# Performance work log

Measured on AMD Instinct MI355X. Metric: run time of the kernel, lower is better.

The kernel has to match this reference:

```python
import jax, jax.numpy as jnp
import numpy as np

H = 16  # n_heads
D = 1024  # embed_dim == input_dim
FF = 4 * D
EPS = 1e-5  # torch LayerNorm default


def layer_norm(x, g, b):
    m = x.mean(-1, keepdims=True)
    v = x.var(-1, keepdims=True)
    return (x - m) / jnp.sqrt(v + EPS) * g + b


def setup_inputs() -> dict:
    key = jax.random.key(0)
    ks = jax.random.split(key, 8)
    s = lambda k, sh: (jax.random.normal(k, sh, jnp.float32) * 0.02)
    return {
        "kq": jax.random.normal(ks[0], (4, 2048, 512), jnp.float32),
        "v": jax.random.normal(ks[1], (4, 2048, 512), jnp.float32),
        "Wk": s(ks[2], (D, D)), "bk": jnp.zeros((D,), jnp.float32),
        "Wq": s(ks[3], (D, D)), "bq": jnp.zeros((D,), jnp.float32),
        "Wv": s(ks[4], (D, D)), "bv": jnp.zeros((D,), jnp.float32),
        "W1": s(ks[5], (FF, D)), "b1": jnp.zeros((FF,), jnp.float32),
        "W2": s(ks[6], (D, FF)), "b2": jnp.zeros((D,), jnp.float32),
        "g1": jnp.ones((D,), jnp.float32), "be1": jnp.zeros((D,), jnp.float32),
        "g2": jnp.ones((D,), jnp.float32), "be2": jnp.zeros((D,), jnp.float32),
    }


def reference(kq, v, Wk, bk, Wq, bq, Wv, bv, W1, b1, W2, b2, g1, be1, g2, be2):
    X = jnp.concatenate([kq, v], axis=-1)  # [n, T, input_dim]
    n, T, _ = kq.shape

    def heads(y):  # [n, T, D] -> [n, H, T, hd]
        return y.reshape(n, T, H, -1).transpose(0, 2, 1, 3)

    K = heads(X @ Wk.T + bk)
    Q = heads(X @ Wq.T + bq)
    V = heads(X @ Wv.T + bv)

    # NOTE: source applies no 1/sqrt(head_dim) scaling
    scores = jnp.einsum('nhqd,nhkd->nhqk', Q, K)
    causal = jnp.tril(jnp.ones((T, T), bool))  # mask = -inf strictly above diagonal
    scores = jnp.where(causal, scores, -jnp.inf)
    A = jax.nn.softmax(scores, axis=-1)
    attn_out = jnp.einsum('nhqk,nhkd->nhqd', A, V)
    attn_out = attn_out.transpose(0, 2, 1, 3).reshape(n, T, -1)  # [n, T, D]

    Vflat = V.transpose(0, 2, 1, 3).reshape(n, T, -1)  # residual is V projection, per source
    h = layer_norm(Vflat + attn_out, g1, be1)
    ff = jax.nn.gelu(h @ W1.T + b1, approximate=False) @ W2.T + b2  # torch GELU default = exact erf
    return layer_norm(h + ff, g2, be2)
```

## Files before the change

### kernel.cpp

```cpp
#include <hip/hip_runtime.h>
#include <stdint.h>

#define SEQ 2048
#define DM  1024
#define NH  16
#define HD  64
#define FFD 4096
#define TOK 8192

typedef __bf16 bf16x8 __attribute__((ext_vector_type(8)));
typedef float  f32x4  __attribute__((ext_vector_type(4)));
typedef float  f32x16 __attribute__((ext_vector_type(16)));
typedef unsigned short u16x8 __attribute__((ext_vector_type(8)));
typedef unsigned short u16x4 __attribute__((ext_vector_type(4)));
typedef unsigned int   u32x4 __attribute__((ext_vector_type(4)));

__device__ __forceinline__ unsigned short f2bf(float f) {
  unsigned u = __builtin_bit_cast(unsigned, f);
  u += 0x7fffu + ((u >> 16) & 1u);
  return (unsigned short)(u >> 16);
}
__device__ __forceinline__ float bf2f(unsigned short h) {
  return __builtin_bit_cast(float, ((unsigned)h) << 16);
}
__device__ __forceinline__ f32x4 mfma16(bf16x8 a, bf16x8 b, f32x4 c) {
  return __builtin_amdgcn_mfma_f32_16x16x32_bf16(a, b, c, 0, 0, 0);
}
__device__ __forceinline__ f32x16 mfma32(bf16x8 a, bf16x8 b, f32x16 c) {
  return __builtin_amdgcn_mfma_f32_32x32x16_bf16(a, b, c, 0, 0, 0);
}
__device__ __forceinline__ unsigned cvtpk(float lo, float hi) {
  unsigned r;
  asm("v_cvt_pk_bf16_f32 %0, %1, %2" : "=v"(r) : "v"(lo), "v"(hi));
  return r;
}
__device__ __forceinline__ void gld_lds16(void* lds, const void* g) {
  __builtin_amdgcn_global_load_lds((__attribute__((address_space(1))) void*)g,
                                   (__attribute__((address_space(3))) void*)lds,
                                   16, 0, 0);
}

__global__ __launch_bounds__(256) void concat_cast(
    const float* __restrict__ kq, const float* __restrict__ v,
    unsigned short* __restrict__ X) {
  int i = (blockIdx.x * 256 + threadIdx.x) * 4;
  int tkn = i >> 10;
  int c = i & 1023;
  const float* s = (c < 512) ? (kq + (size_t)tkn * 512 + c)
                             : (v  + (size_t)tkn * 512 + (c - 512));
  f32x4 f = *(const f32x4*)s;
  u16x4 o = { f2bf(f[0]), f2bf(f[1]), f2bf(f[2]), f2bf(f[3]) };
  *(u16x4*)&X[i] = o;
}

__global__ __launch_bounds__(256) void cast_f2b(
    const float* __restrict__ src, unsigned short* __restrict__ dst, int n) {
  int i = (blockIdx.x * 256 + threadIdx.x) * 4;
  if (i >= n) return;
  f32x4 f = *(const f32x4*)&src[i];
  u16x4 o = { f2bf(f[0]), f2bf(f[1]), f2bf(f[2]), f2bf(f[3]) };
  *(u16x4*)&dst[i] = o;
}

template<int BM, int EPI>
__global__ __launch_bounds__(512, 2) void gemm256(
    const unsigned short* __restrict__ A, const unsigned short* __restrict__ B,
    const float* __restrict__ bias, void* __restrict__ Cout,
    int M, int N, int K) {
  constexpr int MF = BM / 32;
  constexpr int NA = BM / 64;
  constexpr int MQ = MF / 2;
  extern __shared__ __align__(16) unsigned short lds[];
  unsigned short* Asm0 = lds;
  unsigned short* Bsm0 = lds + 2 * BM * 64;
  const int tid = threadIdx.x;
  const int w = tid >> 6, l = tid & 63, lr = l & 15, lg = l >> 4;
  const int wm = w >> 2, wn = w & 3;
  const int nbm = M / BM;
  const int cpx = gridDim.x >> 3;
  const int bid = blockIdx.x;
  const int sw = (bid & 7) * cpx + (bid >> 3);
  const int bm = (sw % nbm) * BM;
  const int bn = (sw / nbm) * 256;
  const int NT = K >> 6;
  const int srow = tid >> 3;
  const int sc8  = tid & 7;

  f32x4 acc[MF][4] = {};

  auto stageA = [&](int kt, int bb) {
    unsigned short* dst = Asm0 + bb * BM * 64;
#pragma unroll
    for (int i = 0; i < NA; ++i) {
      int row = i * 64 + srow;
      gld_lds16(dst + (i * 512 + w * 64) * 8,
                &A[(size_t)(bm + row) * K + kt * 64 + ((sc8 ^ (row & 7)) << 3)]);
    }
  };
  auto stageB = [&](int kt, int bb) {
    unsigned short* dst = Bsm0 + bb * 256 * 64;
#pragma unroll
    for (int i = 0; i < 4; ++i) {
      int row = i * 64 + srow;
      gld_lds16(dst + (i * 512 + w * 64) * 8,
                &B[(size_t)(bn + row) * K + kt * 64 + ((sc8 ^ (row & 7)) << 3)]);
    }
  };

  stageA(0, 0);
  stageB(0, 0);
  __syncthreads();

  for (int t = 0; t < NT; ++t) {
    const int cur = t & 1;
    const bool pre = (t + 1 < NT);
    const unsigned short* As = Asm0 + cur * BM * 64;
    const unsigned short* Bs = Bsm0 + cur * 256 * 64;
#pragma unroll
    for (int q = 0; q < 4; ++q) {
      bf16x8 av[MQ][2], bv[2][2];
#pragma unroll
      for (int fr = 0; fr < MQ; ++fr)
#pragma unroll
        for (int kk = 0; kk < 2; ++kk) {
          int row = wm * (BM / 2) + ((q >> 1) * MQ + fr) * 16 + lr;
          int c8 = (kk * 4 + lg) ^ (row & 7);
          av[fr][kk] = *(const bf16x8*)&As[row * 64 + c8 * 8];
        }
#pragma unroll
      for (int fn = 0; fn < 2; ++fn)
#pragma unroll
        for (int kk = 0; kk < 2; ++kk) {
          int row = wn * 64 + ((q & 1) * 2 + fn) * 16 + lr;
          int c8 = (kk * 4 + lg) ^ (row & 7);
          bv[fn][kk] = *(const bf16x8*)&Bs[row * 64 + c8 * 8];
        }
      if (q == 0 && pre) {
        stageA(t + 1, cur ^ 1);
        if (BM == 128) stageB(t + 1, cur ^ 1);
      }
      if (BM == 256 && q == 1 && pre) stageB(t + 1, cur ^ 1);
      if (q == 3 && pre) asm volatile("s_waitcnt vmcnt(0)" ::: "memory");
      __builtin_amdgcn_s_barrier();
      asm volatile("s_waitcnt lgkmcnt(0)" ::: "memory");
      __builtin_amdgcn_sched_barrier(0);
      __builtin_amdgcn_s_setprio(1);
#pragma unroll
      for (int fr = 0; fr < MQ; ++fr)
#pragma unroll
        for (int fn = 0; fn < 2; ++fn)
#pragma unroll
          for (int kk = 0; kk < 2; ++kk)
            acc[(q >> 1) * MQ + fr][(q & 1) * 2 + fn] =
                mfma16(av[fr][kk], bv[fn][kk],
                       acc[(q >> 1) * MQ + fr][(q & 1) * 2 + fn]);
      __builtin_amdgcn_s_setprio(0);
      __builtin_amdgcn_s_barrier();
    }
  }
#pragma unroll
  for (int mf = 0; mf < MF; ++mf) {
    int row0 = bm + wm * (BM / 2) + mf * 16 + lg * 4;
#pragma unroll
    for (int nf = 0; nf < 4; ++nf) {
      int col = bn + wn * 64 + nf * 16 + lr;
      float bcol = bias[col];
#pragma unroll
      for (int r = 0; r < 4; ++r) {
        float vv = acc[mf][nf][r] + bcol;
        int row = row0 + r;
        if (EPI == 2) vv = 0.5f * vv * (1.0f + erff(vv * 0.70710678118654752f));
        if (EPI == 0)
          ((float*)Cout)[(size_t)row * N + col] = vv;
        else if (EPI == 3) {
          int bb = row >> 11, t = row & 2047;
          int hh = col >> 6, dc = (col >> 4) & 3, dl = col & 15;
          ((unsigned short*)Cout)[((((size_t)(bb * 16 + hh) * 4 + dc) * 2048 + t) << 4) + dl] = f2bf(vv);
        } else
          ((unsigned short*)Cout)[(size_t)row * N + col] = f2bf(vv);
      }
    }
  }
}

__global__ __launch_bounds__(256) void vtrans_kernel(
    const unsigned short* __restrict__ Vb, unsigned short* __restrict__ VI) {
  __shared__ __align__(16) unsigned short T[64][72];
  const int tid = threadIdx.x;
  const int bh = blockIdx.x;
  const int b = bh >> 4, h = bh & 15;
  const int t0 = blockIdx.y * 64;
  const int m = tid & 7;
  const int rr = tid >> 3;
#pragma unroll
  for (int cc = 0; cc < 2; ++cc) {
    int tt = rr + cc * 32;
    u16x8 vv = *(const u16x8*)&Vb[((size_t)b * SEQ + t0 + tt) * DM + h * 64 + m * 8];
    *(u16x8*)&T[tt][(m ^ (tt >> 3)) * 8] = vv;
  }
  __syncthreads();
#pragma unroll
  for (int cc = 0; cc < 2; ++cc) {
    int d = rr + cc * 32;
    u16x8 ov;
#pragma unroll
    for (int jj = 0; jj < 8; ++jj) {
      int tt = m * 8 + jj;
      ov[jj] = T[tt][((d >> 3) ^ (tt >> 3)) * 8 + (d & 7)];
    }
    int kt = (t0 >> 4) + (m >> 1);
    *(u16x8*)&VI[(((size_t)bh * 128 + kt) * 64 + d) * 16 + (m & 1) * 8] = ov;
  }
}

__global__ __launch_bounds__(128, 4) void attn_kernel(
    const unsigned short* __restrict__ Q, const unsigned short* __restrict__ KI,
    const unsigned short* __restrict__ VI, unsigned short* __restrict__ O) {
  __shared__ __align__(16) unsigned short T[2][32 * 72];
  const int tid = threadIdx.x;
  const int w = tid >> 6, l = tid & 63;
  const int q32 = l & 31;
  const int g = l >> 5;
  const int x = blockIdx.x;
  const int bh = (x & 7) * 8 + (x >> 3);
  const int b = bh >> 4, h = bh & 15;
  const int u = 63 - (2 * (int)blockIdx.y + w);
  const size_t tok0 = (size_t)b * SEQ;
  const size_t hoff = (size_t)h * 64;
  const unsigned short* Kp = KI + (size_t)bh * 4 * SEQ * 16;
  const unsigned short* Vp = VI + (size_t)bh * 128 * 64 * 16;

  const int q0 = u * 32;
  const int qg = q0 + q32;

  bf16x8 qf[4];
#pragma unroll
  for (int ks = 0; ks < 4; ++ks)
    qf[ks] = *(const bf16x8*)&Q[(tok0 + qg) * DM + hoff + ks * 16 + g * 8];

  f32x16 ot0 = {}, ot1 = {};
  float m = -3.0e38f, lden = 0.f;

  bf16x8 kf[4], vf[4];
#pragma unroll
  for (int ks = 0; ks < 4; ++ks)
    kf[ks] = *(const bf16x8*)&Kp[((size_t)ks * SEQ + q32) * 16 + g * 8];
#pragma unroll
  for (int dt = 0; dt < 2; ++dt)
#pragma unroll
    for (int s = 0; s < 2; ++s)
      vf[dt * 2 + s] = *(const bf16x8*)&Vp[((size_t)s * 64 + dt * 32 + q32) * 16 + g * 8];

#pragma unroll 1
  for (int j = 0; j <= u; ++j) {
    f32x16 st = {};
    __builtin_amdgcn_s_setprio(1);
#pragma unroll
    for (int ks = 0; ks < 4; ++ks) st = mfma32(kf[ks], qf[ks], st);
    __builtin_amdgcn_s_setprio(0);
    const int jn = (j < u) ? j + 1 : u;
    bf16x8 kn[4], vn[4];
#pragma unroll
    for (int ks = 0; ks < 4; ++ks)
      kn[ks] = *(const bf16x8*)&Kp[((size_t)ks * SEQ + jn * 32 + q32) * 16 + g * 8];
#pragma unroll
    for (int dt = 0; dt < 2; ++dt)
#pragma unroll
      for (int s = 0; s < 2; ++s)
        vn[dt * 2 + s] = *(const bf16x8*)&Vp[(((size_t)jn * 2 + s) * 64 + dt * 32 + q32) * 16 + g * 8];
    if (j == u) {
#pragma unroll
      for (int r = 0; r < 16; ++r) {
        int kg = j * 32 + (r & 3) + 8 * (r >> 2) + 4 * g;
        if (kg > qg) st[r] = -3.0e38f;
      }
    }
    float x0 = fmaxf(st[0], st[1]),  x1 = fmaxf(st[2], st[3]);
    float x2 = fmaxf(st[4], st[5]),  x3 = fmaxf(st[6], st[7]);
    float x4 = fmaxf(st[8], st[9]),  x5 = fmaxf(st[10], st[11]);
    float x6 = fmaxf(st[12], st[13]), x7 = fmaxf(st[14], st[15]);
    x0 = fmaxf(x0, x1); x2 = fmaxf(x2, x3); x4 = fmaxf(x4, x5); x6 = fmaxf(x6, x7);
    x0 = fmaxf(x0, x2); x4 = fmaxf(x4, x6);
    float pmax = fmaxf(x0, x4);
    if (__any(pmax - m > 8.0f)) {
      float pp = fmaxf(pmax, __shfl_xor(pmax, 32, 64));
      float mnew = fmaxf(m, pp);
      float sc = __expf(m - mnew);
#pragma unroll
      for (int r = 0; r < 16; ++r) { ot0[r] *= sc; ot1[r] *= sc; }
      lden *= sc;
      m = mnew;
    }
    float p[16];
#pragma unroll
    for (int r = 0; r < 16; ++r) p[r] = __expf(st[r] - m);
    {
      float s0 = p[0] + p[1], s1 = p[2] + p[3], s2 = p[4] + p[5], s3 = p[6] + p[7];
      float s4 = p[8] + p[9], s5 = p[10] + p[11], s6 = p[12] + p[13], s7 = p[14] + p[15];
      s0 += s1; s2 += s3; s4 += s5; s6 += s7;
      s0 += s2; s4 += s6;
      lden += s0 + s4;
    }
    unsigned c0 = cvtpk(p[0], p[1]),   c1 = cvtpk(p[2], p[3]);
    unsigned c2 = cvtpk(p[4], p[5]),   c3 = cvtpk(p[6], p[7]);
    unsigned c4 = cvtpk(p[8], p[9]),   c5 = cvtpk(p[10], p[11]);
    unsigned c6 = cvtpk(p[12], p[13]), c7 = cvtpk(p[14], p[15]);
    unsigned y0 = __shfl_xor(c0, 32, 64), y1 = __shfl_xor(c1, 32, 64);
    unsigned y2 = __shfl_xor(c2, 32, 64), y3 = __shfl_xor(c3, 32, 64);
    unsigned y4 = __shfl_xor(c4, 32, 64), y5 = __shfl_xor(c5, 32, 64);
    unsigned y6 = __shfl_xor(c6, 32, 64), y7 = __shfl_xor(c7, 32, 64);
    u32x4 f0 = { g ? y2 : c0, g ? y3 : c1, g ? c2 : y0, g ? c3 : y1 };
    u32x4 f1 = { g ? y6 : c4, g ? y7 : c5, g ? c6 : y4, g ? c7 : y5 };
    bf16x8 pb0 = __builtin_bit_cast(bf16x8, f0);
    bf16x8 pb1 = __builtin_bit_cast(bf16x8, f1);
    __builtin_amdgcn_s_setprio(1);
    ot0 = mfma32(vf[0], pb0, ot0);
    ot0 = mfma32(vf[1], pb1, ot0);
    ot1 = mfma32(vf[2], pb0, ot1);
    ot1 = mfma32(vf[3], pb1, ot1);
    __builtin_amdgcn_s_setprio(0);
#pragma unroll
    for (int ks = 0; ks < 4; ++ks) kf[ks] = kn[ks];
#pragma unroll
    for (int q = 0; q < 4; ++q) vf[q] = vn[q];
  }
  lden += __shfl_xor(lden, 32, 64);
  float inv = 1.0f / lden;
#pragma unroll
  for (int r = 0; r < 16; ++r) {
    int d = (r & 3) + 8 * (r >> 2) + 4 * g;
    T[w][q32 * 72 + d]      = f2bf(ot0[r] * inv);
    T[w][q32 * 72 + 32 + d] = f2bf(ot1[r] * inv);
  }
#pragma unroll
  for (int j2 = 0; j2 < 4; ++j2) {
    int col = g * 32 + j2 * 8;
    u16x8 vv = *(const u16x8*)&T[w][q32 * 72 + col];
    *(u16x8*)&O[(tok0 + q0 + q32) * DM + hoff + col] = vv;
  }
}

template<int MODE>
__global__ __launch_bounds__(256) void ln_kernel(
    const unsigned short* __restrict__ Xa, const void* __restrict__ Xc,
    const float* __restrict__ g, const float* __restrict__ be,
    void* __restrict__ outp) {
  const int row = blockIdx.x, t = threadIdx.x;
  const size_t base = (size_t)row * DM + t * 4;
  float x[4];
  u16x4 a = *(const u16x4*)&Xa[base];
  if (MODE == 0) {
    u16x4 c = *(const u16x4*)&((const unsigned short*)Xc)[base];
#pragma unroll
    for (int i = 0; i < 4; ++i) x[i] = bf2f(a[i]) + bf2f(c[i]);
  } else {
    f32x4 c = *(const f32x4*)&((const float*)Xc)[base];
#pragma unroll
    for (int i = 0; i < 4; ++i) x[i] = bf2f(a[i]) + c[i];
  }
  float s = x[0] + x[1] + x[2] + x[3];
  float ss = x[0] * x[0] + x[1] * x[1] + x[2] * x[2] + x[3] * x[3];
#pragma unroll
  for (int m = 1; m < 64; m <<= 1) {
    s  += __shfl_xor(s, m, 64);
    ss += __shfl_xor(ss, m, 64);
  }
  __shared__ float red[8];
  const int w = t >> 6;
  if ((t & 63) == 0) { red[w * 2] = s; red[w * 2 + 1] = ss; }
  __syncthreads();
  s  = red[0] + red[2] + red[4] + red[6];
  ss = red[1] + red[3] + red[5] + red[7];
  const float mean = s * (1.0f / DM);
  const float var = ss * (1.0f / DM) - mean * mean;
  const float rstd = rsqrtf(var + 1e-5f);
  if (MODE == 0) {
    u16x4 o;
#pragma unroll
    for (int i = 0; i < 4; ++i) {
      int cx = t * 4 + i;
      o[i] = f2bf((x[i] - mean) * rstd * g[cx] + be[cx]);
    }
    *(u16x4*)&((unsigned short*)outp)[base] = o;
  } else {
    f32x4 o;
#pragma unroll
    for (int i = 0; i < 4; ++i) {
      int cx = t * 4 + i;
      o[i] = (x[i] - mean) * rstd * g[cx] + be[cx];
    }
    *(f32x4*)&((float*)outp)[base] = o;
  }
}

extern "C" void kernel_launch(void* const* d_in, const int* in_sizes, int n_in,
                              void* d_out, int out_size, void* d_ws, size_t ws_size,
                              hipStream_t stream) {
  (void)in_sizes; (void)n_in; (void)out_size; (void)ws_size;
  const float* kq  = (const float*)d_in[0];
  const float* v   = (const float*)d_in[1];
  const float* Wk  = (const float*)d_in[2];
  const float* bk  = (const float*)d_in[3];
  const float* Wq  = (const float*)d_in[4];
  const float* bq  = (const float*)d_in[5];
  const float* Wv  = (const float*)d_in[6];
  const float* bv  = (const float*)d_in[7];
  const float* W1  = (const float*)d_in[8];
  const float* b1  = (const float*)d_in[9];
  const float* W2  = (const float*)d_in[10];
  const float* b2  = (const float*)d_in[11];
  const float* g1  = (const float*)d_in[12];
  const float* be1 = (const float*)d_in[13];
  const float* g2  = (const float*)d_in[14];
  const float* be2 = (const float*)d_in[15];
  float* out = (float*)d_out;
  uint8_t* ws = (uint8_t*)d_ws;

  unsigned short* Xb  = (unsigned short*)(ws + 0);
  unsigned short* Wkb = (unsigned short*)(ws + 16777216);
  unsigned short* Wqb = (unsigned short*)(ws + 18874368);
  unsigned short* Wvb = (unsigned short*)(ws + 20971520);
  unsigned short* Qb  = (unsigned short*)(ws + 23068672);
  unsigned short* Kb  = (unsigned short*)(ws + 39845888);
  unsigned short* Ab  = (unsigned short*)(ws + 56623104);
  unsigned short* F1b = (unsigned short*)(ws + 0);
  unsigned short* W1b = (unsigned short*)(ws + 73400320);
  unsigned short* W2b = (unsigned short*)(ws + 81788928);
  unsigned short* Vb  = (unsigned short*)(ws + 90177536);
  unsigned short* Hb  = (unsigned short*)(ws + 106954752);
  float*          F2f = (float*)(ws + 123731968);
  unsigned short* VIg = (unsigned short*)(ws + 123731968);

  concat_cast<<<TOK * DM / 1024, 256, 0, stream>>>(kq, v, Xb);
  cast_f2b<<<1024, 256, 0, stream>>>(Wk, Wkb, DM * DM);
  cast_f2b<<<1024, 256, 0, stream>>>(Wq, Wqb, DM * DM);
  cast_f2b<<<1024, 256, 0, stream>>>(Wv, Wvb, DM * DM);
  cast_f2b<<<4096, 256, 0, stream>>>(W1, W1b, FFD * DM);
  cast_f2b<<<4096, 256, 0, stream>>>(W2, W2b, DM * FFD);

  gemm256<128, 3><<<256, 512, 98304, stream>>>(Xb, Wkb, bk, Kb, TOK, DM, DM);
  gemm256<128, 1><<<256, 512, 98304, stream>>>(Xb, Wqb, bq, Qb, TOK, DM, DM);
  gemm256<128, 1><<<256, 512, 98304, stream>>>(Xb, Wvb, bv, Vb, TOK, DM, DM);

  vtrans_kernel<<<dim3(64, 32), 256, 0, stream>>>(Vb, VIg);
  attn_kernel<<<dim3(64, 32), 128, 0, stream>>>(Qb, Kb, VIg, Ab);

  ln_kernel<0><<<TOK, 256, 0, stream>>>(Vb, Ab, g1, be1, Hb);

  gemm256<256, 2><<<512, 512, 131072, stream>>>(Hb, W1b, b1, F1b, TOK, FFD, DM);
  gemm256<128, 0><<<256, 512, 98304, stream>>>(F1b, W2b, b2, F2f, TOK, DM, FFD);

  ln_kernel<1><<<TOK, 256, 0, stream>>>(Hb, F2f, g2, be2, out);
}
```

Baseline: 419.7 us.

## Unify GEMM to 256x256 tiles with a single-barrier double-buffered K loop

Drops the BM template so every GEMM uses 256x256 tiles, and replaces the four sub-phase loop (two barriers per sub-phase with staggered prefetch) with one wait and barrier per K step, followed by a full prefetch of the next tile. B fragments are loaded once per K step and reused across two A groups, which cuts LDS reads and barrier count. The cost is that the QKV and W2 GEMMs now launch only 128 blocks on a 256-CU device, so half the CUs sit idle for those calls. The explicit lgkmcnt wait and sched_barrier are also gone.

```diff
diff --git a/kernel.cpp b/kernel.cpp
--- a/kernel.cpp
+++ b/kernel.cpp
@@ -62,105 +62,83 @@
   *(u16x4*)&dst[i] = o;
 }
 
-template<int BM, int EPI>
+template<int EPI>
 __global__ __launch_bounds__(512, 2) void gemm256(
     const unsigned short* __restrict__ A, const unsigned short* __restrict__ B,
     const float* __restrict__ bias, void* __restrict__ Cout,
     int M, int N, int K) {
-  constexpr int MF = BM / 32;
-  constexpr int NA = BM / 64;
-  constexpr int MQ = MF / 2;
   extern __shared__ __align__(16) unsigned short lds[];
   unsigned short* Asm0 = lds;
-  unsigned short* Bsm0 = lds + 2 * BM * 64;
+  unsigned short* Bsm0 = lds + 2 * 256 * 64;
   const int tid = threadIdx.x;
   const int w = tid >> 6, l = tid & 63, lr = l & 15, lg = l >> 4;
   const int wm = w >> 2, wn = w & 3;
-  const int nbm = M / BM;
+  const int nbm = M >> 8;
   const int cpx = gridDim.x >> 3;
   const int bid = blockIdx.x;
   const int sw = (bid & 7) * cpx + (bid >> 3);
-  const int bm = (sw % nbm) * BM;
-  const int bn = (sw / nbm) * 256;
+  const int bm = (sw % nbm) << 8;
+  const int bn = (sw / nbm) << 8;
   const int NT = K >> 6;
   const int srow = tid >> 3;
   const int sc8  = tid & 7;
 
-  f32x4 acc[MF][4] = {};
-
-  auto stageA = [&](int kt, int bb) {
-    unsigned short* dst = Asm0 + bb * BM * 64;
-#pragma unroll
-    for (int i = 0; i < NA; ++i) {
-      int row = i * 64 + srow;
-      gld_lds16(dst + (i * 512 + w * 64) * 8,
-                &A[(size_t)(bm + row) * K + kt * 64 + ((sc8 ^ (row & 7)) << 3)]);
-    }
-  };
-  auto stageB = [&](int kt, int bb) {
-    unsigned short* dst = Bsm0 + bb * 256 * 64;
+  f32x4 acc[8][4] = {};
+
+  auto stage = [&](int kt, int bb) {
+    unsigned short* da = Asm0 + bb * (256 * 64);
+    unsigned short* db = Bsm0 + bb * (256 * 64);
 #pragma unroll
     for (int i = 0; i < 4; ++i) {
       int row = i * 64 + srow;
-      gld_lds16(dst + (i * 512 + w * 64) * 8,
-                &B[(size_t)(bn + row) * K + kt * 64 + ((sc8 ^ (row & 7)) << 3)]);
+      int c8s = (sc8 ^ (row & 7)) << 3;
+      gld_lds16(da + (i * 512 + w * 64) * 8, &A[(size_t)(bm + row) * K + kt * 64 + c8s]);
+      gld_lds16(db + (i * 512 + w * 64) * 8, &B[(size_t)(bn + row) * K + kt * 64 + c8s]);
     }
   };
 
-  stageA(0, 0);
-  stageB(0, 0);
-  __syncthreads();
+  stage(0, 0);
 
   for (int t = 0; t < NT; ++t) {
-    const int cur = t & 1;
-    const bool pre = (t + 1 < NT);
-    const unsigned short* As = Asm0 + cur * BM * 64;
-    const unsigned short* Bs = Bsm0 + cur * 256 * 64;
-#pragma unroll
-    for (int q = 0; q < 4; ++q) {
-      bf16x8 av[MQ][2], bv[2][2];
-#pragma unroll
-      for (int fr = 0; fr < MQ; ++fr)
+    asm volatile("s_waitcnt vmcnt(0)" ::: "memory");
+    __builtin_amdgcn_s_barrier();
+    if (t + 1 < NT) stage(t + 1, (t + 1) & 1);
+    const unsigned short* As = Asm0 + (t & 1) * (256 * 64);
+    const unsigned short* Bs = Bsm0 + (t & 1) * (256 * 64);
+    bf16x8 bv[4][2];
+#pragma unroll
+    for (int fn = 0; fn < 4; ++fn)
+#pragma unroll
+      for (int kk = 0; kk < 2; ++kk) {
+        int row = wn * 64 + fn * 16 + lr;
+        int c8 = (kk * 4 + lg) ^ (row & 7);
+        bv[fn][kk] = *(const bf16x8*)&Bs[row * 64 + c8 * 8];
+      }
+#pragma unroll
+    for (int mg = 0; mg < 2; ++mg) {
+      bf16x8 av[4][2];
+#pragma unroll
+      for (int fr = 0; fr < 4; ++fr)
 #pragma unroll
         for (int kk = 0; kk < 2; ++kk) {
-          int row = wm * (BM / 2) + ((q >> 1) * MQ + fr) * 16 + lr;
+          int row = wm * 128 + (mg * 4 + fr) * 16 + lr;
           int c8 = (kk * 4 + lg) ^ (row & 7);
           av[fr][kk] = *(const bf16x8*)&As[row * 64 + c8 * 8];
         }
-#pragma unroll
-      for (int fn = 0; fn < 2; ++fn)
-#pragma unroll
-        for (int kk = 0; kk < 2; ++kk) {
-          int row = wn * 64 + ((q & 1) * 2 + fn) * 16 + lr;
-          int c8 = (kk * 4 + lg) ^ (row & 7);
-          bv[fn][kk] = *(const bf16x8*)&Bs[row * 64 + c8 * 8];
-        }
-      if (q == 0 && pre) {
-        stageA(t + 1, cur ^ 1);
-        if (BM == 128) stageB(t + 1, cur ^ 1);
-      }
-      if (BM == 256 && q == 1 && pre) stageB(t + 1, cur ^ 1);
-      if (q == 3 && pre) asm volatile("s_waitcnt vmcnt(0)" ::: "memory");
-      __builtin_amdgcn_s_barrier();
-      asm volatile("s_waitcnt lgkmcnt(0)" ::: "memory");
-      __builtin_amdgcn_sched_barrier(0);
       __builtin_amdgcn_s_setprio(1);
 #pragma unroll
-      for (int fr = 0; fr < MQ; ++fr)
-#pragma unroll
-        for (int fn = 0; fn < 2; ++fn)
+      for (int fr = 0; fr < 4; ++fr)
+#pragma unroll
+        for (int fn = 0; fn < 4; ++fn)
 #pragma unroll
           for (int kk = 0; kk < 2; ++kk)
-            acc[(q >> 1) * MQ + fr][(q & 1) * 2 + fn] =
-                mfma16(av[fr][kk], bv[fn][kk],
-                       acc[(q >> 1) * MQ + fr][(q & 1) * 2 + fn]);
+            acc[mg * 4 + fr][fn] = mfma16(av[fr][kk], bv[fn][kk], acc[mg * 4 + fr][fn]);
       __builtin_amdgcn_s_setprio(0);
-      __builtin_amdgcn_s_barrier();
-    }
-  }
-#pragma unroll
-  for (int mf = 0; mf < MF; ++mf) {
-    int row0 = bm + wm * (BM / 2) + mf * 16 + lg * 4;
+    }
+  }
+#pragma unroll
+  for (int mf = 0; mf < 8; ++mf) {
+    int row0 = bm + wm * 128 + mf * 16 + lg * 4;
 #pragma unroll
     for (int nf = 0; nf < 4; ++nf) {
       int col = bn + wn * 64 + nf * 16 + lr;
@@ -438,17 +416,17 @@
   cast_f2b<<<4096, 256, 0, stream>>>(W1, W1b, FFD * DM);
   cast_f2b<<<4096, 256, 0, stream>>>(W2, W2b, DM * FFD);
 
-  gemm256<128, 3><<<256, 512, 98304, stream>>>(Xb, Wkb, bk, Kb, TOK, DM, DM);
-  gemm256<128, 1><<<256, 512, 98304, stream>>>(Xb, Wqb, bq, Qb, TOK, DM, DM);
-  gemm256<128, 1><<<256, 512, 98304, stream>>>(Xb, Wvb, bv, Vb, TOK, DM, DM);
+  gemm256<3><<<128, 512, 131072, stream>>>(Xb, Wkb, bk, Kb, TOK, DM, DM);
+  gemm256<1><<<128, 512, 131072, stream>>>(Xb, Wqb, bq, Qb, TOK, DM, DM);
+  gemm256<1><<<128, 512, 131072, stream>>>(Xb, Wvb, bv, Vb, TOK, DM, DM);
 
   vtrans_kernel<<<dim3(64, 32), 256, 0, stream>>>(Vb, VIg);
   attn_kernel<<<dim3(64, 32), 128, 0, stream>>>(Qb, Kb, VIg, Ab);
 
   ln_kernel<0><<<TOK, 256, 0, stream>>>(Vb, Ab, g1, be1, Hb);
 
-  gemm256<256, 2><<<512, 512, 131072, stream>>>(Hb, W1b, b1, F1b, TOK, FFD, DM);
-  gemm256<128, 0><<<256, 512, 98304, stream>>>(F1b, W2b, b2, F2f, TOK, DM, FFD);
+  gemm256<2><<<512, 512, 131072, stream>>>(Hb, W1b, b1, F1b, TOK, FFD, DM);
+  gemm256<0><<<128, 512, 131072, stream>>>(F1b, W2b, b2, F2f, TOK, DM, FFD);
 
   ln_kernel<1><<<TOK, 256, 0, stream>>>(Hb, F2f, g2, be2, out);
 }
```

Result: no change. 427.0 us (+1.8%).
